# Kernel optimization log

Measured on AMD Instinct MI355X. Metric: run time of the kernel, lower is better.

## Reference

```python
import jax, jax.numpy as jnp
import numpy as np

B, NV, HID, TDIM = 1024, 256, 256, 128
NODE_IN = 2 + 4 + TDIM  # coords + pos_enc(4) + time_emb


def _sinusoidal_pos_emb(t, dim):
    # standard SinusoidalPosEmb: cat(sin, cos) of t * exp(-i*log(1e4)/(half-1))
    half = dim // 2
    freqs = jnp.exp(-np.log(10000.0) * jnp.arange(half, dtype=t.dtype) / (half - 1))
    ang = t[:, None] * freqs[None, :]
    return jnp.concatenate([jnp.sin(ang), jnp.cos(ang)], axis=-1)  # [B, dim]


def setup_inputs() -> dict:
    key = jax.random.key(0)
    ks = jax.random.split(key, 10)
    s = lambda fan_in: 1.0 / np.sqrt(fan_in)
    return {
        "x": jax.random.normal(ks[0], (B, NV * 2), dtype=jnp.float32),
        "t": jax.random.uniform(ks[1], (B,), dtype=jnp.float32) * 1000.0,
        "time_w": jax.random.normal(ks[2], (TDIM, TDIM), dtype=jnp.float32) * s(TDIM),
        "time_b": jnp.zeros((TDIM,), dtype=jnp.float32),
        "W0": jax.random.normal(ks[3], (NODE_IN, HID), dtype=jnp.float32) * s(NODE_IN),
        "b0": jnp.zeros((HID,), dtype=jnp.float32),
        "W1": jax.random.normal(ks[4], (HID, HID), dtype=jnp.float32) * s(HID),
        "b1": jnp.zeros((HID,), dtype=jnp.float32),
        "W2": jax.random.normal(ks[5], (HID, HID), dtype=jnp.float32) * s(HID),
        "b2": jnp.zeros((HID,), dtype=jnp.float32),
    }


def reference(x, t, time_w, time_b, W0, b0, W1, b1, W2, b2):
    Bsz, D = x.shape
    n = D // 2
    coords = x.reshape(Bsz, n, 2)  # [B, n, 2]

    # cycle positional features (pos_enc_dim=4): sin/cos of vertex angle + 2nd harmonic
    pos = jnp.arange(n, dtype=x.dtype)
    theta = (2.0 * jnp.pi) * pos / n
    pe = jnp.stack([jnp.sin(theta), jnp.cos(theta), jnp.sin(2.0 * theta), jnp.cos(2.0 * theta)], axis=-1)
    pe = jnp.broadcast_to(pe[None], (Bsz, n, 4))

    # time MLP: SinusoidalPosEmb -> Linear -> SiLU, broadcast to every node of the graph
    temb = jax.nn.silu(_sinusoidal_pos_emb(t, time_w.shape[0]) @ time_w + time_b)  # [B, TDIM]
    temb = jnp.broadcast_to(temb[:, None, :], (Bsz, n, temb.shape[-1]))

    h = jnp.concatenate([coords, pe, temb], axis=-1)  # [B, n, NODE_IN]

    # GCN layers over cycle adjacency with self-loops, symmetric-normalized (deg=3 -> 1/3).
    # Cycle structure: neighbors are prev/next vertex within each polygon -> jnp.roll on axis 1.
    for W, b in ((W0, b0), (W1, b1), (W2, b2)):
        s = h @ W + b  # support = x W + b
        agg = (s + jnp.roll(s, 1, axis=1) + jnp.roll(s, -1, axis=1)) / 3.0
        h = jax.nn.silu(agg)

    # mean pooling per graph (scatter_mean over graph_index == mean over vertex axis here)
    return h.mean(axis=1)  # [B, HID]
```

## Files before the change

kernel.cpp:

```cpp
#include <hip/hip_runtime.h>
#include <cstdint>

typedef __attribute__((ext_vector_type(8)))  short bf16x8;
typedef __attribute__((ext_vector_type(16))) float f32x16;
typedef __attribute__((ext_vector_type(4)))  int   i32x4;

__device__ __forceinline__ unsigned short f2bf(float x) {
  unsigned u = __float_as_uint(x);
  u += 0x7fffu + ((u >> 16) & 1u);
  return (unsigned short)(u >> 16);
}
__device__ __forceinline__ unsigned pk2bf(float lo, float hi) {
  unsigned r;
  asm("v_cvt_pk_bf16_f32 %0, %1, %2" : "=v"(r) : "v"(lo), "v"(hi));
  return r;
}
__device__ __forceinline__ float silu_f(float v) {
  return v * __builtin_amdgcn_rcpf(1.0f + __expf(-v));
}

__device__ __forceinline__ float xchg32(float A, float B, int q) {
#if defined(__has_builtin)
#if __has_builtin(__builtin_amdgcn_permlane32_swap)
  auto r = __builtin_amdgcn_permlane32_swap(__float_as_uint(A), __float_as_uint(B),
                                            false, false);
  return __uint_as_float(q ? r[0] : r[1]);
#else
  return __shfl_xor(q ? A : B, 32);
#endif
#else
  return __shfl_xor(q ? A : B, 32);
#endif
}

__global__ void pack_kernel(const float* __restrict__ W0, const float* __restrict__ W1,
                            const float* __restrict__ W2,
                            unsigned short* __restrict__ packW) {
  __shared__ float ldsF[16][257];
  const int s = blockIdx.x, tid = threadIdx.x;
  const float* W; int KT, kmax, base, kt;
  if (s < 9)       { W = W0; KT = 9;  kmax = 134; base = 0;      kt = s; }
  else if (s < 25) { W = W1; KT = 16; kmax = 256; base = 36864;  kt = s - 9; }
  else             { W = W2; KT = 16; kmax = 256; base = 102400; kt = s - 25; }
  const int k0 = kt * 16;
#pragma unroll
  for (int i = 0; i < 8; ++i) {
    const int idx = i * 512 + tid;
    const int kl = idx >> 8, col = idx & 255;
    const int kg = k0 + kl;
    ldsF[kl][col] = (kg < kmax) ? W[kg * 256 + col] * 0.33333334f : 0.0f;
  }
  __syncthreads();
  const int g = tid >> 7, t = (tid >> 6) & 1, lane = tid & 63;
  const int col = g * 64 + t * 32 + (lane & 31);
  const int kb = 8 * (lane >> 5);
  unsigned u0 = pk2bf(ldsF[kb + 0][col], ldsF[kb + 1][col]);
  unsigned u1 = pk2bf(ldsF[kb + 2][col], ldsF[kb + 3][col]);
  unsigned u2 = pk2bf(ldsF[kb + 4][col], ldsF[kb + 5][col]);
  unsigned u3 = pk2bf(ldsF[kb + 6][col], ldsF[kb + 7][col]);
  unsigned short* dst = packW + base + g * (KT * 1024) + t * (KT * 512) + kt * 512 + lane * 8;
  i32x4 v = { (int)u0, (int)u1, (int)u2, (int)u3 };
  *(i32x4*)dst = v;
}


template <int ELAYER, bool DF, bool DL>
__device__ __forceinline__ void epi_pair(
    const int p, const f32x16* accEpi, const int q,
    const float recvI0, const float recvI1, const float recvX,
    const float extP, const float extN,
    const int epiSub, unsigned short* __restrict__ hbuf,
    const int* rowAddr, float& psum) {
  const int t = p >> 3, rp = (p & 7) * 2;
  const float mid = accEpi[t][rp] + accEpi[t][rp + 1];
  float prev, next;
  if (rp > 0) prev = accEpi[t][rp - 1];
  else        prev = q ? (t ? recvI1 : recvI0) : (t ? recvX : extP);
  if (rp < 14) next = accEpi[t][rp + 2];
  else         next = q ? (t ? extN : recvX) : (t ? recvI1 : recvI0);
  const float y0 = silu_f(prev + mid);
  const float y1 = silu_f(mid + next);
  const bool c0 = !(DF && t == 0 && rp == 0 && q == 0);
  const bool c1 = !(DL && t == 1 && rp == 14 && q == 1);
  if constexpr (ELAYER == 2) {
    if (c0) psum += y0;
    if (c1) psum += y1;
  } else {
    const unsigned u = pk2bf(y0, y1);
    char* bp = (char*)hbuf + (2 * epiSub + t) * 16384;
    if (c0) *(unsigned short*)(bp + rowAddr[rp])     = (unsigned short)u;
    if (c1) *(unsigned short*)(bp + rowAddr[rp + 1]) = (unsigned short)(u >> 16);
  }
}

template <int KT, int ELAYER, bool DOEPI, bool DF, bool DL>
__device__ __forceinline__ void fblock(
    unsigned short* __restrict__ hbuf, const int readSub, const int epiSub,
    const bf16x8* Bf, const int q, const int c, const float bias3,
    f32x16* accOut, const f32x16* accEpi,
    const float extP, const float extN,
    const int* rowAddr, float& psum) {
  float recvI0 = 0.f, recvI1 = 0.f, recvX = 0.f;
  if constexpr (DOEPI) {
    recvI0 = xchg32(accEpi[0][0],  accEpi[0][15], q);
    recvI1 = xchg32(accEpi[1][0],  accEpi[1][15], q);
    recvX  = xchg32(accEpi[0][15], accEpi[1][0],  q);
  }
#pragma unroll
  for (int t2 = 0; t2 < 2; ++t2)
#pragma unroll
    for (int j = 0; j < 16; ++j) accOut[t2][j] = bias3;
  const unsigned short* rb = hbuf + readSub * 16384 + c * 256;
  bf16x8 a0 = *(const bf16x8*)(rb + ((q ^ c) * 8));
  bf16x8 a1 = *(const bf16x8*)(rb + ((q ^ c) * 8) + 8192);
#pragma unroll
  for (int kt = 0; kt < KT; ++kt) {
    const bf16x8 u0 = a0, u1 = a1;
    if (kt + 1 < KT) {
      const unsigned short* nb = rb + (((2 * (kt + 1) + q) ^ c) * 8);
      a0 = *(const bf16x8*)(nb);
      a1 = *(const bf16x8*)(nb + 8192);
    }
    accOut[0] = __builtin_amdgcn_mfma_f32_32x32x16_bf16(u0, Bf[kt], accOut[0], 0, 0, 0);
    accOut[1] = __builtin_amdgcn_mfma_f32_32x32x16_bf16(u1, Bf[kt], accOut[1], 0, 0, 0);
    if constexpr (DOEPI) {
#pragma unroll
      for (int p = (kt * 16) / KT; p < ((kt + 1) * 16) / KT; ++p)
        epi_pair<ELAYER, DF, DL>(p, accEpi, q, recvI0, recvI1, recvX, extP, extN,
                                 epiSub, hbuf, rowAddr, psum);
    }
  }
}

template <int ELAYER>
__device__ __forceinline__ void epi_only(
    const f32x16* accEpi, const int q, const float extP, const float extN,
    const int epiSub, unsigned short* __restrict__ hbuf,
    const int* rowAddr, float& psum) {
  const float recvI0 = xchg32(accEpi[0][0],  accEpi[0][15], q);
  const float recvI1 = xchg32(accEpi[1][0],  accEpi[1][15], q);
  const float recvX  = xchg32(accEpi[0][15], accEpi[1][0],  q);
#pragma unroll
  for (int p = 0; p < 16; ++p)
    epi_pair<ELAYER, false, false>(p, accEpi, q, recvI0, recvI1, recvX, extP, extN,
                                   epiSub, hbuf, rowAddr, psum);
}

template <int ELAYER>
__device__ __forceinline__ void defer_last(
    const f32x16* accEpi, const float accNew00, const int epiSub,
    const int q, unsigned short* __restrict__ hbuf,
    const int* rowAddr, float& psum) {
  const float recv = xchg32(0.f, accNew00, q);
  const float y = silu_f(accEpi[1][14] + accEpi[1][15] + recv);
  if (q) {
    if constexpr (ELAYER == 2) psum += y;
    else *(unsigned short*)((char*)hbuf + (2 * epiSub + 1) * 16384 + rowAddr[15]) = f2bf(y);
  }
}

template <int ELAYER>
__device__ __forceinline__ void fix_node0(
    const float s255src, const float sv0, const float sv1,
    const int q, unsigned short* __restrict__ hbuf,
    const int* rowAddr, float& psum) {
  const float recv = xchg32(s255src, 0.f, q);
  const float y = silu_f(recv + sv0 + sv1);
  if (!q) {
    if constexpr (ELAYER == 2) psum += y;
    else *(unsigned short*)((char*)hbuf + rowAddr[0]) = f2bf(y);
  }
}

__global__ __launch_bounds__(512, 1) void poly_kernel(
    const float* __restrict__ x, const float* __restrict__ t,
    const float* __restrict__ tw, const float* __restrict__ tb,
    const unsigned short* __restrict__ packW,
    const float* __restrict__ B0, const float* __restrict__ B1,
    const float* __restrict__ B2, float* __restrict__ out) {
  __shared__ __align__(16) unsigned short hbuf[65536];
  __shared__ __align__(16) unsigned short tmpl[160];

  const int tid = threadIdx.x;
  const int w = tid >> 6, lane = tid & 63, q = lane >> 5, c = lane & 31;
  const int b = blockIdx.x;

  {
    float* scr = (float*)hbuf;
    if (tid < 128) {
      const float tv = t[b];
      const int i = tid & 63;
      const float f = expf(-0.14619588396823767f * (float)i);
      const float ang = tv * f;
      scr[tid] = (tid < 64) ? sinf(ang) : cosf(ang);
    }
    __syncthreads();
    {
      const int j = tid & 127, p = tid >> 7;
      float a = 0.f;
#pragma unroll 8
      for (int kk = 0; kk < 32; ++kk) a += scr[p * 32 + kk] * tw[(p * 32 + kk) * 128 + j];
      scr[128 + tid] = a;
    }
    __syncthreads();
    if (tid < 128) {
      const float a = tb[tid] + scr[128 + tid] + scr[256 + tid] + scr[384 + tid] + scr[512 + tid];
      tmpl[6 + tid] = f2bf(silu_f(a));
      if (tid < 6)  tmpl[tid] = 0;
      if (tid < 26) tmpl[134 + tid] = 0;
    }
    __syncthreads();
  }

  const unsigned short* pL0 = packW + (w >> 1) * (9 * 1024) + (w & 1) * (9 * 512);
  const unsigned short* pL1 = packW + 36864 + (w >> 1) * (16 * 1024) + (w & 1) * (16 * 512);
  const unsigned short* pL2 = packW + 102400 + (w >> 1) * (16 * 1024) + (w & 1) * (16 * 512);
  bf16x8 Bf[16];
#pragma unroll
  for (int kt = 0; kt < 9; ++kt) Bf[kt] = *(const bf16x8*)(pL0 + kt * 512 + lane * 8);
  const float b30 = B0[w * 32 + c] * 0.33333334f;
  const float b31 = B1[w * 32 + c] * 0.33333334f;
  const float b32 = B2[w * 32 + c] * 0.33333334f;

  float initL0;
  {
    f32x16 Ct;
#pragma unroll
    for (int j = 0; j < 16; ++j) Ct[j] = 0.f;
#pragma unroll
    for (int kt = 0; kt < 9; ++kt) {
      const bf16x8 at = *(const bf16x8*)(tmpl + kt * 16 + q * 8);
      Ct = __builtin_amdgcn_mfma_f32_32x32x16_bf16(at, Bf[kt], Ct, 0, 0, 0);
    }
    initL0 = Ct[0] + b30;
  }

  {
    const int node = tid >> 1, sl = tid & 1;
    i32x4 d = {0, 0, 0, 0};
    if (sl == 0) {
      const float2 xy = ((const float2*)x)[b * 256 + node];
      const float th = 0.024543692605870074f * (float)node;
      d.x = (int)pk2bf(xy.x, xy.y);
      d.y = (int)pk2bf(sinf(th), cosf(th));
      d.z = (int)pk2bf(sinf(2.f * th), cosf(2.f * th));
    }
    const int m = (node & 3) + 8 * ((node >> 2) & 3) + 4 * ((node >> 4) & 1);
    const int R = (node & ~31) | m;
    *(i32x4*)(hbuf + R * 256 + ((sl ^ m) * 8)) = d;
  }

  int rowAddr[16];
  const int slotW = 4 * w + (c >> 3), offW = (c & 7) * 2;
#pragma unroll
  for (int r = 0; r < 16; ++r) {
    const int row = (r & 3) + 8 * (r >> 2) + 4 * q;
    rowAddr[r] = row * 512 + ((slotW ^ row) * 16) + offW;
  }
  __syncthreads();

  f32x16 accA[2], accB[2];
  float psum = 0.f, sv0, sv1, extP, extN;

  fblock<1, 0, false, false, false>(hbuf, 0, 0, Bf, q, c, initL0, accA, accA, 0.f, 0.f, rowAddr, psum);
  sv0 = accA[0][0]; sv1 = accA[0][1];
  __syncthreads();
  fblock<1, 0, true, true, true>(hbuf, 1, 0, Bf, q, c, initL0, accB, accA, 0.f, 0.f, rowAddr, psum);
  defer_last<0>(accA, accB[0][0], 0, q, hbuf, rowAddr, psum);
  extP = xchg32(accA[1][15], 0.f, q);
  __syncthreads();
  fblock<1, 0, true, false, true>(hbuf, 2, 1, Bf, q, c, initL0, accA, accB, extP, 0.f, rowAddr, psum);
  defer_last<0>(accB, accA[0][0], 1, q, hbuf, rowAddr, psum);
  extP = xchg32(accB[1][15], 0.f, q);
  __syncthreads();
  fblock<1, 0, true, false, true>(hbuf, 3, 2, Bf, q, c, initL0, accB, accA, extP, 0.f, rowAddr, psum);
#pragma unroll
  for (int kt = 0; kt < 16; ++kt) Bf[kt] = *(const bf16x8*)(pL1 + kt * 512 + lane * 8);
  defer_last<0>(accA, accB[0][0], 2, q, hbuf, rowAddr, psum);
  fix_node0<0>(accB[1][15], sv0, sv1, q, hbuf, rowAddr, psum);
  extP = xchg32(accA[1][15], 0.f, q);
  extN = xchg32(0.f, sv0, q);
  __syncthreads();

  fblock<16, 0, true, false, false>(hbuf, 0, 3, Bf, q, c, b31, accA, accB, extP, extN, rowAddr, psum);
  sv0 = accA[0][0]; sv1 = accA[0][1];
  __syncthreads();
  fblock<16, 1, true, true, true>(hbuf, 1, 0, Bf, q, c, b31, accB, accA, 0.f, 0.f, rowAddr, psum);
  defer_last<1>(accA, accB[0][0], 0, q, hbuf, rowAddr, psum);
  extP = xchg32(accA[1][15], 0.f, q);
  __syncthreads();
  fblock<16, 1, true, false, true>(hbuf, 2, 1, Bf, q, c, b31, accA, accB, extP, 0.f, rowAddr, psum);
  defer_last<1>(accB, accA[0][0], 1, q, hbuf, rowAddr, psum);
  extP = xchg32(accB[1][15], 0.f, q);
  __syncthreads();
  fblock<16, 1, true, false, true>(hbuf, 3, 2, Bf, q, c, b31, accB, accA, extP, 0.f, rowAddr, psum);
#pragma unroll
  for (int kt = 0; kt < 16; ++kt) Bf[kt] = *(const bf16x8*)(pL2 + kt * 512 + lane * 8);
  defer_last<1>(accA, accB[0][0], 2, q, hbuf, rowAddr, psum);
  fix_node0<1>(accB[1][15], sv0, sv1, q, hbuf, rowAddr, psum);
  extP = xchg32(accA[1][15], 0.f, q);
  extN = xchg32(0.f, sv0, q);
  __syncthreads();

  fblock<16, 1, true, false, false>(hbuf, 0, 3, Bf, q, c, b32, accA, accB, extP, extN, rowAddr, psum);
  sv0 = accA[0][0]; sv1 = accA[0][1];
  __syncthreads();
  fblock<16, 2, true, true, true>(hbuf, 1, 0, Bf, q, c, b32, accB, accA, 0.f, 0.f, rowAddr, psum);
  defer_last<2>(accA, accB[0][0], 0, q, hbuf, rowAddr, psum);
  extP = xchg32(accA[1][15], 0.f, q);
  fblock<16, 2, true, false, true>(hbuf, 2, 1, Bf, q, c, b32, accA, accB, extP, 0.f, rowAddr, psum);
  defer_last<2>(accB, accA[0][0], 1, q, hbuf, rowAddr, psum);
  extP = xchg32(accB[1][15], 0.f, q);
  fblock<16, 2, true, false, true>(hbuf, 3, 2, Bf, q, c, b32, accB, accA, extP, 0.f, rowAddr, psum);
  defer_last<2>(accA, accB[0][0], 2, q, hbuf, rowAddr, psum);
  fix_node0<2>(accB[1][15], sv0, sv1, q, hbuf, rowAddr, psum);
  extP = xchg32(accA[1][15], 0.f, q);
  extN = xchg32(0.f, sv0, q);
  epi_only<2>(accB, q, extP, extN, 3, hbuf, rowAddr, psum);

  const float s2 = psum + xchg32(psum, psum, q);
  if (q == 0) out[b * 256 + w * 32 + c] = s2 * (1.0f / 256.0f);
}

extern "C" void kernel_launch(void* const* d_in, const int* in_sizes, int n_in,
                              void* d_out, int out_size, void* d_ws, size_t ws_size,
                              hipStream_t stream) {
  const float* x  = (const float*)d_in[0];
  const float* t  = (const float*)d_in[1];
  const float* tw = (const float*)d_in[2];
  const float* tb = (const float*)d_in[3];
  const float* W0 = (const float*)d_in[4];
  const float* b0 = (const float*)d_in[5];
  const float* W1 = (const float*)d_in[6];
  const float* b1 = (const float*)d_in[7];
  const float* W2 = (const float*)d_in[8];
  const float* b2 = (const float*)d_in[9];

  unsigned short* packW = (unsigned short*)d_ws;
  float* out = (float*)d_out;

  pack_kernel<<<41, 512, 0, stream>>>(W0, W1, W2, packW);
  poly_kernel<<<1024, 512, 0, stream>>>(x, t, tw, tb, packW, b0, b1, b2, out);
}
```

Before: 174.3 us.

## Process 128-node halves per block step instead of 64-node quarters

The per-layer software pipeline changes from four 64-node sub-blocks (two 32-row MFMA tiles each) to two 128-node halves (four tiles each). Each weight fragment in registers now feeds four MFMAs, and the number of block barriers and deferred boundary fix-ups per layer is halved. In exchange the accumulator register footprint doubles, from four to eight f32x16 tiles, and the explicit A-operand prefetch from LDS is removed, so more register pressure and less load latency hiding are possible.

```diff
diff --git a/kernel.cpp b/kernel.cpp
--- a/kernel.cpp
+++ b/kernel.cpp
@@ -64,109 +64,104 @@
 }
 
 
-template <int ELAYER, bool DF, bool DL>
-__device__ __forceinline__ void epi_pair(
-    const int p, const f32x16* accEpi, const int q,
-    const float recvI0, const float recvI1, const float recvX,
-    const float extP, const float extN,
-    const int epiSub, unsigned short* __restrict__ hbuf,
+__device__ __forceinline__ f32x16 MF(const bf16x8 a, const bf16x8 b, const f32x16 c) {
+  return __builtin_amdgcn_mfma_f32_32x32x16_bf16(a, b, c, 0, 0, 0);
+}
+
+template <int ELAYER, bool DEFER>
+__device__ __forceinline__ void epi_pairP(
+    const int p, const f32x16* aO, const int q,
+    const float* I, const float* X, const float extP, const float extN,
+    const int epiPair, unsigned short* __restrict__ hbuf,
     const int* rowAddr, float& psum) {
-  const int t = p >> 3, rp = (p & 7) * 2;
-  const float mid = accEpi[t][rp] + accEpi[t][rp + 1];
+  const int tt = p >> 3, rp = (p & 7) * 2;
+  const float mid = aO[tt][rp] + aO[tt][rp + 1];
   float prev, next;
-  if (rp > 0) prev = accEpi[t][rp - 1];
-  else        prev = q ? (t ? recvI1 : recvI0) : (t ? recvX : extP);
-  if (rp < 14) next = accEpi[t][rp + 2];
-  else         next = q ? (t ? extN : recvX) : (t ? recvI1 : recvI0);
+  if (rp > 0) prev = aO[tt][rp - 1];
+  else        prev = q ? I[tt] : (tt == 0 ? extP : X[tt - 1]);
+  if (rp < 14) next = aO[tt][rp + 2];
+  else         next = q ? (tt == 3 ? extN : X[tt]) : I[tt];
   const float y0 = silu_f(prev + mid);
   const float y1 = silu_f(mid + next);
-  const bool c0 = !(DF && t == 0 && rp == 0 && q == 0);
-  const bool c1 = !(DL && t == 1 && rp == 14 && q == 1);
+  const bool c0 = !(DEFER && tt == 0 && rp == 0 && q == 0);
+  const bool c1 = !(DEFER && tt == 3 && rp == 14 && q == 1);
   if constexpr (ELAYER == 2) {
     if (c0) psum += y0;
     if (c1) psum += y1;
   } else {
     const unsigned u = pk2bf(y0, y1);
-    char* bp = (char*)hbuf + (2 * epiSub + t) * 16384;
+    char* bp = (char*)hbuf + (epiPair * 4 + tt) * 16384;
     if (c0) *(unsigned short*)(bp + rowAddr[rp])     = (unsigned short)u;
     if (c1) *(unsigned short*)(bp + rowAddr[rp + 1]) = (unsigned short)(u >> 16);
   }
 }
 
-template <int KT, int ELAYER, bool DOEPI, bool DF, bool DL>
-__device__ __forceinline__ void fblock(
-    unsigned short* __restrict__ hbuf, const int readSub, const int epiSub,
+template <int KT, int ELAYER, bool DOEPI, bool DEFER>
+__device__ __forceinline__ void fblockP(
+    unsigned short* __restrict__ hbuf, const int readPair, const int epiPair,
     const bf16x8* Bf, const int q, const int c, const float bias3,
-    f32x16* accOut, const f32x16* accEpi,
-    const float extP, const float extN,
+    f32x16* aN, const f32x16* aO, const float extP, const float extN,
     const int* rowAddr, float& psum) {
-  float recvI0 = 0.f, recvI1 = 0.f, recvX = 0.f;
+  float I[4], X[3];
   if constexpr (DOEPI) {
-    recvI0 = xchg32(accEpi[0][0],  accEpi[0][15], q);
-    recvI1 = xchg32(accEpi[1][0],  accEpi[1][15], q);
-    recvX  = xchg32(accEpi[0][15], accEpi[1][0],  q);
-  }
-#pragma unroll
-  for (int t2 = 0; t2 < 2; ++t2)
-#pragma unroll
-    for (int j = 0; j < 16; ++j) accOut[t2][j] = bias3;
-  const unsigned short* rb = hbuf + readSub * 16384 + c * 256;
-  bf16x8 a0 = *(const bf16x8*)(rb + ((q ^ c) * 8));
-  bf16x8 a1 = *(const bf16x8*)(rb + ((q ^ c) * 8) + 8192);
+#pragma unroll
+    for (int tt = 0; tt < 4; ++tt) I[tt] = xchg32(aO[tt][0], aO[tt][15], q);
+#pragma unroll
+    for (int tt = 0; tt < 3; ++tt) X[tt] = xchg32(aO[tt][15], aO[tt + 1][0], q);
+  }
+#pragma unroll
+  for (int tt = 0; tt < 4; ++tt)
+#pragma unroll
+    for (int j = 0; j < 16; ++j) aN[tt][j] = bias3;
+  const unsigned short* rb = hbuf + readPair * 32768 + c * 256;
 #pragma unroll
   for (int kt = 0; kt < KT; ++kt) {
-    const bf16x8 u0 = a0, u1 = a1;
-    if (kt + 1 < KT) {
-      const unsigned short* nb = rb + (((2 * (kt + 1) + q) ^ c) * 8);
-      a0 = *(const bf16x8*)(nb);
-      a1 = *(const bf16x8*)(nb + 8192);
-    }
-    accOut[0] = __builtin_amdgcn_mfma_f32_32x32x16_bf16(u0, Bf[kt], accOut[0], 0, 0, 0);
-    accOut[1] = __builtin_amdgcn_mfma_f32_32x32x16_bf16(u1, Bf[kt], accOut[1], 0, 0, 0);
+    const unsigned short* ap = rb + (((2 * kt + q) ^ c) * 8);
+    const bf16x8 a0 = *(const bf16x8*)(ap);
+    const bf16x8 a1 = *(const bf16x8*)(ap + 8192);
+    const bf16x8 a2 = *(const bf16x8*)(ap + 16384);
+    const bf16x8 a3 = *(const bf16x8*)(ap + 24576);
+    aN[0] = MF(a0, Bf[kt], aN[0]);
+    aN[1] = MF(a1, Bf[kt], aN[1]);
+    aN[2] = MF(a2, Bf[kt], aN[2]);
+    aN[3] = MF(a3, Bf[kt], aN[3]);
     if constexpr (DOEPI) {
 #pragma unroll
-      for (int p = (kt * 16) / KT; p < ((kt + 1) * 16) / KT; ++p)
-        epi_pair<ELAYER, DF, DL>(p, accEpi, q, recvI0, recvI1, recvX, extP, extN,
-                                 epiSub, hbuf, rowAddr, psum);
+      for (int p = (kt * 32) / KT; p < ((kt + 1) * 32) / KT; ++p)
+        epi_pairP<ELAYER, DEFER>(p, aO, q, I, X, extP, extN, epiPair,
+                                 hbuf, rowAddr, psum);
     }
   }
 }
 
 template <int ELAYER>
-__device__ __forceinline__ void epi_only(
-    const f32x16* accEpi, const int q, const float extP, const float extN,
-    const int epiSub, unsigned short* __restrict__ hbuf,
+__device__ __forceinline__ void epi_onlyP(
+    const f32x16* aO, const int q, const float extP, const float extN,
+    const int epiPair, unsigned short* __restrict__ hbuf,
     const int* rowAddr, float& psum) {
-  const float recvI0 = xchg32(accEpi[0][0],  accEpi[0][15], q);
-  const float recvI1 = xchg32(accEpi[1][0],  accEpi[1][15], q);
-  const float recvX  = xchg32(accEpi[0][15], accEpi[1][0],  q);
-#pragma unroll
-  for (int p = 0; p < 16; ++p)
-    epi_pair<ELAYER, false, false>(p, accEpi, q, recvI0, recvI1, recvX, extP, extN,
-                                   epiSub, hbuf, rowAddr, psum);
+  float I[4], X[3];
+#pragma unroll
+  for (int tt = 0; tt < 4; ++tt) I[tt] = xchg32(aO[tt][0], aO[tt][15], q);
+#pragma unroll
+  for (int tt = 0; tt < 3; ++tt) X[tt] = xchg32(aO[tt][15], aO[tt + 1][0], q);
+#pragma unroll
+  for (int p = 0; p < 32; ++p)
+    epi_pairP<ELAYER, false>(p, aO, q, I, X, extP, extN, epiPair,
+                             hbuf, rowAddr, psum);
 }
 
 template <int ELAYER>
-__device__ __forceinline__ void defer_last(
-    const f32x16* accEpi, const float accNew00, const int epiSub,
-    const int q, unsigned short* __restrict__ hbuf,
-    const int* rowAddr, float& psum) {
-  const float recv = xchg32(0.f, accNew00, q);
-  const float y = silu_f(accEpi[1][14] + accEpi[1][15] + recv);
+__device__ __forceinline__ void fixesP(
+    const f32x16* aA, const f32x16* aB, const int q,
+    unsigned short* __restrict__ hbuf, const int* rowAddr, float& psum) {
+  const float r128 = xchg32(0.f, aB[0][0], q);
+  const float r255 = xchg32(aB[3][15], 0.f, q);
   if (q) {
+    const float y = silu_f(aA[3][14] + aA[3][15] + r128);
     if constexpr (ELAYER == 2) psum += y;
-    else *(unsigned short*)((char*)hbuf + (2 * epiSub + 1) * 16384 + rowAddr[15]) = f2bf(y);
-  }
-}
-
-template <int ELAYER>
-__device__ __forceinline__ void fix_node0(
-    const float s255src, const float sv0, const float sv1,
-    const int q, unsigned short* __restrict__ hbuf,
-    const int* rowAddr, float& psum) {
-  const float recv = xchg32(s255src, 0.f, q);
-  const float y = silu_f(recv + sv0 + sv1);
-  if (!q) {
+    else *(unsigned short*)((char*)hbuf + 3 * 16384 + rowAddr[15]) = f2bf(y);
+  } else {
+    const float y = silu_f(r255 + aA[0][0] + aA[0][1]);
     if constexpr (ELAYER == 2) psum += y;
     else *(unsigned short*)((char*)hbuf + rowAddr[0]) = f2bf(y);
   }
@@ -218,7 +213,6 @@
   bf16x8 Bf[16];
 #pragma unroll
   for (int kt = 0; kt < 9; ++kt) Bf[kt] = *(const bf16x8*)(pL0 + kt * 512 + lane * 8);
-  const float b30 = B0[w * 32 + c] * 0.33333334f;
   const float b31 = B1[w * 32 + c] * 0.33333334f;
   const float b32 = B2[w * 32 + c] * 0.33333334f;
 
@@ -230,9 +224,9 @@
 #pragma unroll
     for (int kt = 0; kt < 9; ++kt) {
       const bf16x8 at = *(const bf16x8*)(tmpl + kt * 16 + q * 8);
-      Ct = __builtin_amdgcn_mfma_f32_32x32x16_bf16(at, Bf[kt], Ct, 0, 0, 0);
-    }
-    initL0 = Ct[0] + b30;
+      Ct = MF(at, Bf[kt], Ct);
+    }
+    initL0 = Ct[0] + B0[w * 32 + c] * 0.33333334f;
   }
 
   {
@@ -259,64 +253,36 @@
   }
   __syncthreads();
 
-  f32x16 accA[2], accB[2];
-  float psum = 0.f, sv0, sv1, extP, extN;
-
-  fblock<1, 0, false, false, false>(hbuf, 0, 0, Bf, q, c, initL0, accA, accA, 0.f, 0.f, rowAddr, psum);
-  sv0 = accA[0][0]; sv1 = accA[0][1];
-  __syncthreads();
-  fblock<1, 0, true, true, true>(hbuf, 1, 0, Bf, q, c, initL0, accB, accA, 0.f, 0.f, rowAddr, psum);
-  defer_last<0>(accA, accB[0][0], 0, q, hbuf, rowAddr, psum);
-  extP = xchg32(accA[1][15], 0.f, q);
-  __syncthreads();
-  fblock<1, 0, true, false, true>(hbuf, 2, 1, Bf, q, c, initL0, accA, accB, extP, 0.f, rowAddr, psum);
-  defer_last<0>(accB, accA[0][0], 1, q, hbuf, rowAddr, psum);
-  extP = xchg32(accB[1][15], 0.f, q);
-  __syncthreads();
-  fblock<1, 0, true, false, true>(hbuf, 3, 2, Bf, q, c, initL0, accB, accA, extP, 0.f, rowAddr, psum);
+  f32x16 accA[4], accB[4];
+  float psum = 0.f, extP, extN;
+
+  fblockP<1, 0, false, false>(hbuf, 0, 0, Bf, q, c, initL0, accA, accA, 0.f, 0.f, rowAddr, psum);
+  __syncthreads();
+  fblockP<1, 0, true, true>(hbuf, 1, 0, Bf, q, c, initL0, accB, accA, 0.f, 0.f, rowAddr, psum);
 #pragma unroll
   for (int kt = 0; kt < 16; ++kt) Bf[kt] = *(const bf16x8*)(pL1 + kt * 512 + lane * 8);
-  defer_last<0>(accA, accB[0][0], 2, q, hbuf, rowAddr, psum);
-  fix_node0<0>(accB[1][15], sv0, sv1, q, hbuf, rowAddr, psum);
-  extP = xchg32(accA[1][15], 0.f, q);
-  extN = xchg32(0.f, sv0, q);
-  __syncthreads();
-
-  fblock<16, 0, true, false, false>(hbuf, 0, 3, Bf, q, c, b31, accA, accB, extP, extN, rowAddr, psum);
-  sv0 = accA[0][0]; sv1 = accA[0][1];
-  __syncthreads();
-  fblock<16, 1, true, true, true>(hbuf, 1, 0, Bf, q, c, b31, accB, accA, 0.f, 0.f, rowAddr, psum);
-  defer_last<1>(accA, accB[0][0], 0, q, hbuf, rowAddr, psum);
-  extP = xchg32(accA[1][15], 0.f, q);
-  __syncthreads();
-  fblock<16, 1, true, false, true>(hbuf, 2, 1, Bf, q, c, b31, accA, accB, extP, 0.f, rowAddr, psum);
-  defer_last<1>(accB, accA[0][0], 1, q, hbuf, rowAddr, psum);
-  extP = xchg32(accB[1][15], 0.f, q);
-  __syncthreads();
-  fblock<16, 1, true, false, true>(hbuf, 3, 2, Bf, q, c, b31, accB, accA, extP, 0.f, rowAddr, psum);
+  fixesP<0>(accA, accB, q, hbuf, rowAddr, psum);
+  __syncthreads();
+
+  extP = xchg32(accA[3][15], 0.f, q);
+  extN = xchg32(0.f, accA[0][0], q);
+  fblockP<16, 0, true, false>(hbuf, 0, 1, Bf, q, c, b31, accA, accB, extP, extN, rowAddr, psum);
+  __syncthreads();
+  fblockP<16, 1, true, true>(hbuf, 1, 0, Bf, q, c, b31, accB, accA, 0.f, 0.f, rowAddr, psum);
 #pragma unroll
   for (int kt = 0; kt < 16; ++kt) Bf[kt] = *(const bf16x8*)(pL2 + kt * 512 + lane * 8);
-  defer_last<1>(accA, accB[0][0], 2, q, hbuf, rowAddr, psum);
-  fix_node0<1>(accB[1][15], sv0, sv1, q, hbuf, rowAddr, psum);
-  extP = xchg32(accA[1][15], 0.f, q);
-  extN = xchg32(0.f, sv0, q);
-  __syncthreads();
-
-  fblock<16, 1, true, false, false>(hbuf, 0, 3, Bf, q, c, b32, accA, accB, extP, extN, rowAddr, psum);
-  sv0 = accA[0][0]; sv1 = accA[0][1];
-  __syncthreads();
-  fblock<16, 2, true, true, true>(hbuf, 1, 0, Bf, q, c, b32, accB, accA, 0.f, 0.f, rowAddr, psum);
-  defer_last<2>(accA, accB[0][0], 0, q, hbuf, rowAddr, psum);
-  extP = xchg32(accA[1][15], 0.f, q);
-  fblock<16, 2, true, false, true>(hbuf, 2, 1, Bf, q, c, b32, accA, accB, extP, 0.f, rowAddr, psum);
-  defer_last<2>(accB, accA[0][0], 1, q, hbuf, rowAddr, psum);
-  extP = xchg32(accB[1][15], 0.f, q);
-  fblock<16, 2, true, false, true>(hbuf, 3, 2, Bf, q, c, b32, accB, accA, extP, 0.f, rowAddr, psum);
-  defer_last<2>(accA, accB[0][0], 2, q, hbuf, rowAddr, psum);
-  fix_node0<2>(accB[1][15], sv0, sv1, q, hbuf, rowAddr, psum);
-  extP = xchg32(accA[1][15], 0.f, q);
-  extN = xchg32(0.f, sv0, q);
-  epi_only<2>(accB, q, extP, extN, 3, hbuf, rowAddr, psum);
+  fixesP<1>(accA, accB, q, hbuf, rowAddr, psum);
+  __syncthreads();
+
+  extP = xchg32(accA[3][15], 0.f, q);
+  extN = xchg32(0.f, accA[0][0], q);
+  fblockP<16, 1, true, false>(hbuf, 0, 1, Bf, q, c, b32, accA, accB, extP, extN, rowAddr, psum);
+  __syncthreads();
+  fblockP<16, 2, true, true>(hbuf, 1, 0, Bf, q, c, b32, accB, accA, 0.f, 0.f, rowAddr, psum);
+  fixesP<2>(accA, accB, q, hbuf, rowAddr, psum);
+  extP = xchg32(accA[3][15], 0.f, q);
+  extN = xchg32(0.f, accA[0][0], q);
+  epi_onlyP<2>(accB, q, extP, extN, 1, hbuf, rowAddr, psum);
 
   const float s2 = psum + xchg32(psum, psum, q);
   if (q == 0) out[b * 256 + w * 32 + c] = s2 * (1.0f / 256.0f);
```

New measurement: 176.8 us. Within noise of the previous version (+1.4%).
